# Performance work log

Measured on AMD Instinct MI355X. Metric: run time of the kernel, lower is better.

The kernel has to match this reference:

```python
import jax, jax.numpy as jnp
import numpy as np

N_NODES = 50000
N_EDGES = 800000


def _gcn_conv(x, src, dst, norm, W, b, num_nodes):
    # x: [N, Fin] -> h: [N, Fout]; messages gathered from src, scattered to dst.
    h = x @ W
    msgs = h[src] * norm[:, None]                      # [E+N, Fout]
    out = jax.ops.segment_sum(msgs, dst, num_segments=num_nodes)
    return out + b


def _gcn_norm(edge_index, num_nodes):
    # Add self-loops and compute symmetric normalization D^-1/2 (A+I) D^-1/2.
    loops = jnp.arange(num_nodes, dtype=edge_index.dtype)
    src = jnp.concatenate([edge_index[0], loops])
    dst = jnp.concatenate([edge_index[1], loops])
    ones = jnp.ones(src.shape[0], dtype=jnp.float32)
    deg = jax.ops.segment_sum(ones, dst, num_segments=num_nodes)
    dinv = jnp.where(deg > 0, jax.lax.rsqrt(jnp.maximum(deg, 1.0)), 0.0)
    norm = dinv[src] * dinv[dst]
    return src, dst, norm


def setup_inputs() -> dict:
    key = jax.random.key(0)
    k1, k2, k3, k4 = jax.random.split(key, 4)
    map_x = jax.random.normal(k1, (N_NODES, 128), dtype=jnp.float32)
    edge_index = jax.random.randint(k2, (2, N_EDGES), 0, N_NODES, dtype=jnp.int64)
    W1 = jax.random.normal(k3, (128, 64), dtype=jnp.float32) * (1.0 / np.sqrt(128))
    b1 = jnp.zeros((64,), dtype=jnp.float32)
    W2 = jax.random.normal(k4, (64, 32), dtype=jnp.float32) * (1.0 / np.sqrt(64))
    b2 = jnp.zeros((32,), dtype=jnp.float32)
    return {"map": map_x, "edge_index": edge_index, "W1": W1, "b1": b1, "W2": W2, "b2": b2}


def reference(map, edge_index, W1, b1, W2, b2):
    num_nodes = map.shape[0]
    src, dst, norm = _gcn_norm(edge_index, num_nodes)
    x = jax.nn.relu(_gcn_conv(map, src, dst, norm, W1, b1, num_nodes))
    x = jax.nn.relu(_gcn_conv(x, src, dst, norm, W2, b2, num_nodes))
    return x
```

## Files before the change

### kernel.cpp

```cpp
#include <hip/hip_runtime.h>

#define TPB 256
#define ACHUNK 4096
#define BSHIFT 6
#define BNODES 64
#define CAP 2048
#define GROWS 128

__device__ __forceinline__ float blo(unsigned u) { return __uint_as_float(u << 16); }
__device__ __forceinline__ float bhi(unsigned u) { return __uint_as_float(u & 0xffff0000u); }
__device__ __forceinline__ unsigned pack2(float a, float b) {
    unsigned ua = __float_as_uint(a); ua += 0x7fffu + ((ua >> 16) & 1u);
    unsigned ub = __float_as_uint(b); ub += 0x7fffu + ((ub >> 16) & 1u);
    return (ua >> 16) | (ub & 0xffff0000u);
}
__device__ __forceinline__ void dec8(uint4 v, float* f) {
    f[0] = blo(v.x); f[1] = bhi(v.x); f[2] = blo(v.y); f[3] = bhi(v.y);
    f[4] = blo(v.z); f[5] = bhi(v.z); f[6] = blo(v.w); f[7] = bhi(v.w);
}
__device__ __forceinline__ void dec4(uint2 v, float* f) {
    f[0] = blo(v.x); f[1] = bhi(v.x); f[2] = blo(v.y); f[3] = bhi(v.y);
}


__global__ __launch_bounds__(TPB) void k_fat(
        const int* __restrict__ src, const int* __restrict__ dst, int E,
        int* __restrict__ bcnt, int* __restrict__ tmp, int NB,
        const float* __restrict__ X, const float* __restrict__ W,
        unsigned int* __restrict__ H1b, int N, int G1, int FB) {
    __shared__ float Ws[128 * 64];
    int* lcnt = (int*)Ws;
    int bid = blockIdx.x;
    int t = threadIdx.x;

    if ((bid % 3) == 0) {
        int fidx = bid / 3;
        if (fidx >= FB) return;
        int c0 = fidx * ACHUNK;
        int s_[16], d_[16];
#pragma unroll
        for (int i = 0; i < 16; i++) {
            int e = c0 + i * TPB + t;
            if (e < E) { s_[i] = src[e]; d_[i] = dst[e]; }
            else d_[i] = -1;
        }
        for (int b = t; b < NB; b += TPB) lcnt[b] = 0;
        __syncthreads();
#pragma unroll
        for (int i = 0; i < 16; i++)
            if (d_[i] >= 0) atomicAdd(&lcnt[d_[i] >> BSHIFT], 1);
        __syncthreads();
        for (int b = t; b < NB; b += TPB) {
            int c = lcnt[b];
            lcnt[b] = c ? (b * CAP + atomicAdd(&bcnt[b], c)) : 0;
        }
        __syncthreads();
#pragma unroll
        for (int i = 0; i < 16; i++) {
            if (d_[i] >= 0) {
                int bkt = d_[i] >> BSHIFT;
                int pos = atomicAdd(&lcnt[bkt], 1);
                if (pos < (bkt + 1) * CAP) {
                    tmp[pos] = ((d_[i] & (BNODES - 1)) << 16) | s_[i];
                }
            }
        }
    } else {
        int gb = bid - bid / 3 - 1;
        if (gb >= G1) return;
        int row0 = gb * GROWS;

        const float4* W4 = (const float4*)W;
        float4* Ws4 = (float4*)Ws;
#pragma unroll
        for (int i = 0; i < 8; i++) Ws4[t + i * 256] = W4[t + i * 256];
        __syncthreads();

        int rg = t >> 3;
        int c0 = (t & 7) * 8;
        int r0 = row0 + rg * 4;
        int ri[4];
#pragma unroll
        for (int i = 0; i < 4; i++) ri[i] = (r0 + i < N) ? (r0 + i) : (N - 1);

        float acc[4][8];
#pragma unroll
        for (int i = 0; i < 4; i++)
#pragma unroll
            for (int j = 0; j < 8; j++) acc[i][j] = 0.0f;

        const float4* X4 = (const float4*)X;
        for (int kk = 0; kk < 32; kk++) {
            float4 xv[4];
#pragma unroll
            for (int i = 0; i < 4; i++) xv[i] = X4[(size_t)ri[i] * 32 + kk];
#pragma unroll
            for (int q = 0; q < 4; q++) {
                const float* w = Ws + (4 * kk + q) * 64 + c0;
                float wq[8];
#pragma unroll
                for (int j = 0; j < 8; j++) wq[j] = w[j];
                float xq[4];
                xq[0] = q == 0 ? xv[0].x : q == 1 ? xv[0].y : q == 2 ? xv[0].z : xv[0].w;
                xq[1] = q == 0 ? xv[1].x : q == 1 ? xv[1].y : q == 2 ? xv[1].z : xv[1].w;
                xq[2] = q == 0 ? xv[2].x : q == 1 ? xv[2].y : q == 2 ? xv[2].z : xv[2].w;
                xq[3] = q == 0 ? xv[3].x : q == 1 ? xv[3].y : q == 2 ? xv[3].z : xv[3].w;
#pragma unroll
                for (int i = 0; i < 4; i++)
#pragma unroll
                    for (int j = 0; j < 8; j++)
                        acc[i][j] = fmaf(xq[i], wq[j], acc[i][j]);
            }
        }
#pragma unroll
        for (int i = 0; i < 4; i++) {
            if (r0 + i < N) {
                uint4 p = { pack2(acc[i][0], acc[i][1]), pack2(acc[i][2], acc[i][3]),
                            pack2(acc[i][4], acc[i][5]), pack2(acc[i][6], acc[i][7]) };
                *(uint4*)(H1b + (size_t)(r0 + i) * 32 + (t & 7) * 4) = p;
            }
        }
    }
}


__global__ __launch_bounds__(TPB) void k_csr(
        const int* __restrict__ bcnt, const int* __restrict__ tmp,
        int* __restrict__ rowptr, unsigned short* __restrict__ rowlen,
        float* __restrict__ dinv, unsigned short* __restrict__ edges, int N) {
    __shared__ int hist[BNODES];
    __shared__ int cur[BNODES];
    __shared__ int sh[BNODES];
    int b = blockIdx.x;
    int t = threadIdx.x;
    int node0 = b << BSHIFT;
    int nn = N - node0; if (nn > BNODES) nn = BNODES;
    int cnt = bcnt[b]; if (cnt > CAP) cnt = CAP;
    const int tb = b * CAP;

    int v[8];
#pragma unroll
    for (int i = 0; i < 8; i++) {
        int idx = t + i * TPB;
        v[i] = (idx < cnt) ? tmp[tb + idx] : -1;
    }
    if (t < BNODES) hist[t] = 0;
    __syncthreads();
#pragma unroll
    for (int i = 0; i < 8; i++)
        if (v[i] >= 0) atomicAdd(&hist[v[i] >> 16], 1);
    __syncthreads();
    if (t < BNODES) sh[t] = (hist[t] + 7) & ~7;
    __syncthreads();
    for (int o = 1; o < BNODES; o <<= 1) {
        int x = (t >= o && t < BNODES) ? sh[t - o] : 0;
        __syncthreads();
        if (t < BNODES) sh[t] += x;
        __syncthreads();
    }
    if (t < BNODES) {
        int len = hist[t];
        int excl = sh[t] - ((len + 7) & ~7);
        cur[t] = excl;
        float dv = rsqrtf((float)(len + 1));
        if (t < nn) {
            dinv[node0 + t] = dv;
            rowptr[node0 + t] = tb + excl;
            rowlen[node0 + t] = (unsigned short)len;
        }
    }
    __syncthreads();
#pragma unroll
    for (int i = 0; i < 8; i++) {
        if (v[i] >= 0) {
            int pos = atomicAdd(&cur[v[i] >> 16], 1);
            if (pos < CAP)
                edges[tb + pos] = (unsigned short)(v[i] & 0xffff);
        }
    }
}


__global__ __launch_bounds__(TPB) void k_gg(
        const int* __restrict__ rowptr, const unsigned short* __restrict__ rowlen,
        const unsigned short* __restrict__ edges,
        const unsigned int* __restrict__ h1b,
        const float* __restrict__ dinv, const float* __restrict__ b1,
        const float* __restrict__ W2, unsigned int* __restrict__ g2b, int N) {
    __shared__ float W2s[64 * 32];
    __shared__ float rows[32 * 68];
    __shared__ float dl[32];
    __shared__ int nst[32];
    __shared__ int nlen[32];
    int t = threadIdx.x;
    int node0 = blockIdx.x * 32;
    int nn = N - node0; if (nn > 32) nn = 32;
    if (nn <= 0) return;

    {
        const float4* W4 = (const float4*)W2;
        float4* Wd = (float4*)W2s;
        Wd[t] = W4[t]; Wd[t + 256] = W4[t + 256];
    }
    if (t < nn) {
        dl[t] = dinv[node0 + t];
        nst[t] = rowptr[node0 + t];
        nlen[t] = rowlen[node0 + t];
    }
    __syncthreads();

    const uint4* G4 = (const uint4*)h1b;
    int nl = t >> 3;
    int lane = t & 7;
    if (nl < nn) {
        float acc[8], f[8];
        float w0 = dl[nl];
        uint4 sv = G4[(size_t)(node0 + nl) * 8 + lane];
        dec8(sv, f);
#pragma unroll
        for (int k = 0; k < 8; k++) acc[k] = w0 * f[k];
        int base = nst[nl], deg = nlen[nl];
        int j = 0;
        for (; j + 7 < deg; j += 8) {
            uint4 ev = *(const uint4*)(edges + base + j);
            int s[8];
            s[0] = ev.x & 0xffff; s[1] = ev.x >> 16;
            s[2] = ev.y & 0xffff; s[3] = ev.y >> 16;
            s[4] = ev.z & 0xffff; s[5] = ev.z >> 16;
            s[6] = ev.w & 0xffff; s[7] = ev.w >> 16;
            uint4 r[8]; float dv[8];
#pragma unroll
            for (int u = 0; u < 8; u++) {
                r[u] = G4[(size_t)s[u] * 8 + lane];
                dv[u] = dinv[s[u]];
            }
#pragma unroll
            for (int u = 0; u < 8; u++) {
                dec8(r[u], f);
#pragma unroll
                for (int k = 0; k < 8; k++) acc[k] = fmaf(dv[u], f[k], acc[k]);
            }
        }
        for (; j < deg; j++) {
            int s0 = edges[base + j];
            float dvx = dinv[s0];
            uint4 r0 = G4[(size_t)s0 * 8 + lane];
            dec8(r0, f);
#pragma unroll
            for (int k = 0; k < 8; k++) acc[k] = fmaf(dvx, f[k], acc[k]);
        }
        const float4* bb4 = (const float4*)(b1 + lane * 8);
        float4 ba = bb4[0], bc = bb4[1];
        float* rr = rows + nl * 68 + lane * 8;
        rr[0] = fmaxf(fmaf(acc[0], w0, ba.x), 0.0f);
        rr[1] = fmaxf(fmaf(acc[1], w0, ba.y), 0.0f);
        rr[2] = fmaxf(fmaf(acc[2], w0, ba.z), 0.0f);
        rr[3] = fmaxf(fmaf(acc[3], w0, ba.w), 0.0f);
        rr[4] = fmaxf(fmaf(acc[4], w0, bc.x), 0.0f);
        rr[5] = fmaxf(fmaf(acc[5], w0, bc.y), 0.0f);
        rr[6] = fmaxf(fmaf(acc[6], w0, bc.z), 0.0f);
        rr[7] = fmaxf(fmaf(acc[7], w0, bc.w), 0.0f);
    }
    __syncthreads();

    int n = t >> 3;
    int c = t & 7;
    if (n < nn) {
        const float* row = rows + n * 68;
        float a0 = 0.0f, a1 = 0.0f, a2 = 0.0f, a3 = 0.0f;
#pragma unroll 8
        for (int k = 0; k < 64; k++) {
            float rv = row[k];
            const float* w = W2s + k * 32 + 4 * c;
            a0 = fmaf(rv, w[0], a0); a1 = fmaf(rv, w[1], a1);
            a2 = fmaf(rv, w[2], a2); a3 = fmaf(rv, w[3], a3);
        }
        float dv = dl[n];
        uint2 p = { pack2(a0 * dv, a1 * dv), pack2(a2 * dv, a3 * dv) };
        ((uint2*)g2b)[(size_t)(node0 + n) * 8 + c] = p;
    }
}


__global__ __launch_bounds__(TPB) void k_g32(
        const int* __restrict__ rowptr, const unsigned short* __restrict__ rowlen,
        const unsigned short* __restrict__ edges,
        const unsigned int* __restrict__ g2b,
        const float* __restrict__ dinv, const float* __restrict__ b2,
        float* __restrict__ out, int N) {
    __shared__ float dl[32];
    __shared__ int nst[32];
    __shared__ int nlen[32];
    int t = threadIdx.x;
    int node0 = blockIdx.x * 32;
    int nn = N - node0; if (nn > 32) nn = 32;
    if (nn <= 0) return;
    if (t < nn) {
        dl[t] = dinv[node0 + t];
        nst[t] = rowptr[node0 + t];
        nlen[t] = rowlen[node0 + t];
    }
    __syncthreads();

    int nl = t >> 3;
    int lane = t & 7;
    if (nl >= nn) return;

    const uint2* G2 = (const uint2*)g2b;
    float acc[4], f[4];
    uint2 sv = G2[(size_t)(node0 + nl) * 8 + lane];
    dec4(sv, acc);
    int base = nst[nl], deg = nlen[nl];
    int j = 0;
    for (; j + 15 < deg; j += 16) {
        uint4 ea = *(const uint4*)(edges + base + j);
        uint4 eb = *(const uint4*)(edges + base + j + 8);
        int s[16];
        s[0]  = ea.x & 0xffff; s[1]  = ea.x >> 16; s[2]  = ea.y & 0xffff; s[3]  = ea.y >> 16;
        s[4]  = ea.z & 0xffff; s[5]  = ea.z >> 16; s[6]  = ea.w & 0xffff; s[7]  = ea.w >> 16;
        s[8]  = eb.x & 0xffff; s[9]  = eb.x >> 16; s[10] = eb.y & 0xffff; s[11] = eb.y >> 16;
        s[12] = eb.z & 0xffff; s[13] = eb.z >> 16; s[14] = eb.w & 0xffff; s[15] = eb.w >> 16;
        uint2 r[16];
#pragma unroll
        for (int u = 0; u < 16; u++) r[u] = G2[(size_t)s[u] * 8 + lane];
#pragma unroll
        for (int u = 0; u < 16; u++) {
            dec4(r[u], f);
            acc[0] += f[0]; acc[1] += f[1]; acc[2] += f[2]; acc[3] += f[3];
        }
    }
    for (; j + 7 < deg; j += 8) {
        uint4 ea = *(const uint4*)(edges + base + j);
        int s[8];
        s[0] = ea.x & 0xffff; s[1] = ea.x >> 16; s[2] = ea.y & 0xffff; s[3] = ea.y >> 16;
        s[4] = ea.z & 0xffff; s[5] = ea.z >> 16; s[6] = ea.w & 0xffff; s[7] = ea.w >> 16;
        uint2 r[8];
#pragma unroll
        for (int u = 0; u < 8; u++) r[u] = G2[(size_t)s[u] * 8 + lane];
#pragma unroll
        for (int u = 0; u < 8; u++) {
            dec4(r[u], f);
            acc[0] += f[0]; acc[1] += f[1]; acc[2] += f[2]; acc[3] += f[3];
        }
    }
    for (; j < deg; j++) {
        uint2 r0 = G2[(size_t)edges[base + j] * 8 + lane];
        dec4(r0, f);
        acc[0] += f[0]; acc[1] += f[1]; acc[2] += f[2]; acc[3] += f[3];
    }
    float w0 = dl[nl];
    const float4* bb4 = (const float4*)(b2 + lane * 4);
    float4 ba = bb4[0];
    float4 o0 = { fmaxf(fmaf(acc[0], w0, ba.x), 0.0f),
                  fmaxf(fmaf(acc[1], w0, ba.y), 0.0f),
                  fmaxf(fmaf(acc[2], w0, ba.z), 0.0f),
                  fmaxf(fmaf(acc[3], w0, ba.w), 0.0f) };
    *(float4*)(out + (size_t)(node0 + nl) * 32 + lane * 4) = o0;
}

static inline int cdiv(int a, int b) { return (a + b - 1) / b; }
static inline char* alignup(char* p) { return (char*)(((uintptr_t)p + 255) & ~(uintptr_t)255); }

extern "C" void kernel_launch(void* const* d_in, const int* in_sizes, int n_in,
                              void* d_out, int out_size, void* d_ws, size_t ws_size,
                              hipStream_t stream) {
    const float* x  = (const float*)d_in[0];
    const int*   ei = (const int*)d_in[1];
    const float* W1 = (const float*)d_in[2];
    const float* b1 = (const float*)d_in[3];
    const float* W2 = (const float*)d_in[4];
    const float* b2 = (const float*)d_in[5];
    float* out = (float*)d_out;

    int N = in_sizes[0] / 128;
    int E = in_sizes[1] / 2;
    const int* src = ei;
    const int* dst = ei + E;

    int NB = cdiv(N, BNODES);

    char* p = (char*)d_ws;
    float* dinv  = (float*)p;            p = alignup(p + sizeof(float) * N);
    int* rowptr  = (int*)p;              p = alignup(p + sizeof(int) * N);
    unsigned short* rowlen = (unsigned short*)p;  p = alignup(p + sizeof(short) * N);
    int* bcnt    = (int*)p;              p = alignup(p + sizeof(int) * 1024);
    int* tmp     = (int*)p;              p = alignup(p + sizeof(int) * (size_t)NB * CAP);
    unsigned short* edges = (unsigned short*)p;   p = alignup(p + sizeof(short) * (size_t)NB * CAP);
    unsigned int* h1b = (unsigned int*)p; p = alignup(p + sizeof(short) * (size_t)N * 64);
    unsigned int* g2b = (unsigned int*)p; p = alignup(p + sizeof(short) * (size_t)N * 32);

    dim3 blk(TPB);
    int FB = cdiv(E, ACHUNK);
    int G1 = cdiv(N, GROWS);
    int fat = 1;
    while ((fat + 2) / 3 < FB || fat - (fat + 2) / 3 < G1) fat++;

    hipMemsetAsync(bcnt, 0, sizeof(int) * 1024, stream);
    k_fat<<<fat, blk, 0, stream>>>(src, dst, E, bcnt, tmp, NB,
                                   x, W1, h1b, N, G1, FB);
    k_csr<<<NB, blk, 0, stream>>>(bcnt, tmp, rowptr, rowlen, dinv, edges, N);
    k_gg<<<cdiv(N, 32), blk, 0, stream>>>(rowptr, rowlen, edges, h1b,
                                          dinv, b1, W2, g2b, N);
    k_g32<<<cdiv(N, 32), blk, 0, stream>>>(rowptr, rowlen, edges, g2b,
                                           dinv, b2, out, N);
}
```

Baseline: 149.1 us.

## Fuse all GCN stages into one cooperative persistent kernel with grid syncs

Replaces the memset and four separate launches with a single cooperative kernel that loops over work items and uses grid-wide barriers between the bucketing/GEMM, CSR build, layer-1 gather, and layer-2 gather phases. Bucketing now writes per-chunk partitioned slots with private counts instead of global atomics on a shared counter, so no memset is needed and the CSR phase concatenates the chunk slices. This removes launch gaps and global atomics but adds grid.sync overhead and a persistent grid whose size comes from an occupancy query. The per-chunk cap of 64 edges per bucket could truncate edges on skewed inputs.

New measurement: 409.1 us. 174% more time.

```diff
diff --git a/kernel.cpp b/kernel.cpp
--- a/kernel.cpp
+++ b/kernel.cpp
@@ -1,11 +1,16 @@
 #include <hip/hip_runtime.h>
+#include <hip/hip_cooperative_groups.h>
+
+namespace cg = cooperative_groups;
 
 #define TPB 256
-#define ACHUNK 4096
+#define EPB 16384
 #define BSHIFT 6
 #define BNODES 64
+#define PCAP 64
 #define CAP 2048
 #define GROWS 128
+#define SMEMB 36864
 
 __device__ __forceinline__ float blo(unsigned u) { return __uint_as_float(u << 16); }
 __device__ __forceinline__ float bhi(unsigned u) { return __uint_as_float(u & 0xffff0000u); }
@@ -23,339 +28,361 @@
 }
 
 
-__global__ __launch_bounds__(TPB) void k_fat(
+__global__ __launch_bounds__(TPB, 4) void k_all(
         const int* __restrict__ src, const int* __restrict__ dst, int E,
-        int* __restrict__ bcnt, int* __restrict__ tmp, int NB,
-        const float* __restrict__ X, const float* __restrict__ W,
-        unsigned int* __restrict__ H1b, int N, int G1, int FB) {
-    __shared__ float Ws[128 * 64];
-    int* lcnt = (int*)Ws;
-    int bid = blockIdx.x;
-    int t = threadIdx.x;
-
-    if ((bid % 3) == 0) {
-        int fidx = bid / 3;
-        if (fidx >= FB) return;
-        int c0 = fidx * ACHUNK;
-        int s_[16], d_[16];
-#pragma unroll
-        for (int i = 0; i < 16; i++) {
-            int e = c0 + i * TPB + t;
-            if (e < E) { s_[i] = src[e]; d_[i] = dst[e]; }
-            else d_[i] = -1;
-        }
-        for (int b = t; b < NB; b += TPB) lcnt[b] = 0;
+        const float* __restrict__ X, const float* __restrict__ W1,
+        const float* __restrict__ b1, const float* __restrict__ W2,
+        const float* __restrict__ b2,
+        unsigned short* __restrict__ cnt, int* __restrict__ tmp,
+        float* __restrict__ dinv, int* __restrict__ rowptr,
+        unsigned short* __restrict__ rowlen, unsigned short* __restrict__ edges,
+        unsigned int* __restrict__ h1b, unsigned int* __restrict__ g2b,
+        float* __restrict__ out,
+        int N, int NB, int FB, int G1, int FAT, int NT) {
+    __shared__ __align__(16) char smem[SMEMB];
+    cg::grid_group grid = cg::this_grid();
+    const int t = threadIdx.x;
+    const int bid = blockIdx.x;
+    const int G = gridDim.x;
+
+    for (int w = bid; w < FAT; w += G) {
         __syncthreads();
-#pragma unroll
-        for (int i = 0; i < 16; i++)
-            if (d_[i] >= 0) atomicAdd(&lcnt[d_[i] >> BSHIFT], 1);
-        __syncthreads();
-        for (int b = t; b < NB; b += TPB) {
-            int c = lcnt[b];
-            lcnt[b] = c ? (b * CAP + atomicAdd(&bcnt[b], c)) : 0;
-        }
-        __syncthreads();
-#pragma unroll
-        for (int i = 0; i < 16; i++) {
-            if (d_[i] >= 0) {
-                int bkt = d_[i] >> BSHIFT;
-                int pos = atomicAdd(&lcnt[bkt], 1);
-                if (pos < (bkt + 1) * CAP) {
-                    tmp[pos] = ((d_[i] & (BNODES - 1)) << 16) | s_[i];
-                }
-            }
-        }
-    } else {
-        int gb = bid - bid / 3 - 1;
-        if (gb >= G1) return;
-        int row0 = gb * GROWS;
-
-        const float4* W4 = (const float4*)W;
-        float4* Ws4 = (float4*)Ws;
-#pragma unroll
-        for (int i = 0; i < 8; i++) Ws4[t + i * 256] = W4[t + i * 256];
-        __syncthreads();
-
-        int rg = t >> 3;
-        int c0 = (t & 7) * 8;
-        int r0 = row0 + rg * 4;
-        int ri[4];
-#pragma unroll
-        for (int i = 0; i < 4; i++) ri[i] = (r0 + i < N) ? (r0 + i) : (N - 1);
-
-        float acc[4][8];
-#pragma unroll
-        for (int i = 0; i < 4; i++)
-#pragma unroll
-            for (int j = 0; j < 8; j++) acc[i][j] = 0.0f;
-
-        const float4* X4 = (const float4*)X;
-        for (int kk = 0; kk < 32; kk++) {
-            float4 xv[4];
-#pragma unroll
-            for (int i = 0; i < 4; i++) xv[i] = X4[(size_t)ri[i] * 32 + kk];
-#pragma unroll
-            for (int q = 0; q < 4; q++) {
-                const float* w = Ws + (4 * kk + q) * 64 + c0;
-                float wq[8];
-#pragma unroll
-                for (int j = 0; j < 8; j++) wq[j] = w[j];
-                float xq[4];
-                xq[0] = q == 0 ? xv[0].x : q == 1 ? xv[0].y : q == 2 ? xv[0].z : xv[0].w;
-                xq[1] = q == 0 ? xv[1].x : q == 1 ? xv[1].y : q == 2 ? xv[1].z : xv[1].w;
-                xq[2] = q == 0 ? xv[2].x : q == 1 ? xv[2].y : q == 2 ? xv[2].z : xv[2].w;
-                xq[3] = q == 0 ? xv[3].x : q == 1 ? xv[3].y : q == 2 ? xv[3].z : xv[3].w;
+        if (w % 3 == 0) {
+            int k = w / 3;
+            if (k < FB) {
+                unsigned short* dstl = (unsigned short*)smem;
+                int* hist = (int*)(smem + 32768);
+                int e0 = k * EPB;
+                int ne = E - e0; if (ne > EPB) ne = EPB;
+                for (int b = t; b < NB; b += TPB) hist[b] = 0;
+                __syncthreads();
+                for (int i = t; i < ne; i += TPB) {
+                    int d = dst[e0 + i];
+                    dstl[i] = (unsigned short)d;
+                    atomicAdd(&hist[d >> BSHIFT], 1);
+                }
+                __syncthreads();
+                for (int b = t; b < NB; b += TPB) {
+                    int c = hist[b]; if (c > PCAP) c = PCAP;
+                    cnt[k * NB + b] = (unsigned short)c;
+                    hist[b] = (k * NB + b) * PCAP;
+                }
+                __syncthreads();
+                for (int i = t; i < ne; i += TPB) {
+                    int s = src[e0 + i];
+                    int d = dstl[i];
+                    int b = d >> BSHIFT;
+                    int pos = atomicAdd(&hist[b], 1);
+                    if (pos < (k * NB + b + 1) * PCAP)
+                        tmp[pos] = ((d & (BNODES - 1)) << 16) | s;
+                }
+            }
+        } else {
+            int gb = w - w / 3 - 1;
+            if (gb < G1) {
+                float* Ws = (float*)smem;
+                const float4* W4 = (const float4*)W1;
+                float4* Ws4 = (float4*)Ws;
+#pragma unroll
+                for (int i = 0; i < 8; i++) Ws4[t + i * 256] = W4[t + i * 256];
+                __syncthreads();
+
+                int row0 = gb * GROWS;
+                int rg = t >> 3;
+                int c0 = (t & 7) * 8;
+                int r0 = row0 + rg * 4;
+                int ri[4];
+#pragma unroll
+                for (int i = 0; i < 4; i++) ri[i] = (r0 + i < N) ? (r0 + i) : (N - 1);
+
+                float acc[4][8];
 #pragma unroll
                 for (int i = 0; i < 4; i++)
 #pragma unroll
-                    for (int j = 0; j < 8; j++)
-                        acc[i][j] = fmaf(xq[i], wq[j], acc[i][j]);
-            }
-        }
-#pragma unroll
-        for (int i = 0; i < 4; i++) {
-            if (r0 + i < N) {
-                uint4 p = { pack2(acc[i][0], acc[i][1]), pack2(acc[i][2], acc[i][3]),
-                            pack2(acc[i][4], acc[i][5]), pack2(acc[i][6], acc[i][7]) };
-                *(uint4*)(H1b + (size_t)(r0 + i) * 32 + (t & 7) * 4) = p;
+                    for (int j = 0; j < 8; j++) acc[i][j] = 0.0f;
+
+                const float4* X4 = (const float4*)X;
+                for (int kk = 0; kk < 32; kk++) {
+                    float4 xv[4];
+#pragma unroll
+                    for (int i = 0; i < 4; i++) xv[i] = X4[(size_t)ri[i] * 32 + kk];
+#pragma unroll
+                    for (int q = 0; q < 4; q++) {
+                        const float* ww = Ws + (4 * kk + q) * 64 + c0;
+                        float wq[8];
+#pragma unroll
+                        for (int j = 0; j < 8; j++) wq[j] = ww[j];
+                        float xq[4];
+                        xq[0] = q == 0 ? xv[0].x : q == 1 ? xv[0].y : q == 2 ? xv[0].z : xv[0].w;
+                        xq[1] = q == 0 ? xv[1].x : q == 1 ? xv[1].y : q == 2 ? xv[1].z : xv[1].w;
+                        xq[2] = q == 0 ? xv[2].x : q == 1 ? xv[2].y : q == 2 ? xv[2].z : xv[2].w;
+                        xq[3] = q == 0 ? xv[3].x : q == 1 ? xv[3].y : q == 2 ? xv[3].z : xv[3].w;
+#pragma unroll
+                        for (int i = 0; i < 4; i++)
+#pragma unroll
+                            for (int j = 0; j < 8; j++)
+                                acc[i][j] = fmaf(xq[i], wq[j], acc[i][j]);
+                    }
+                }
+#pragma unroll
+                for (int i = 0; i < 4; i++) {
+                    if (r0 + i < N) {
+                        uint4 p = { pack2(acc[i][0], acc[i][1]), pack2(acc[i][2], acc[i][3]),
+                                    pack2(acc[i][4], acc[i][5]), pack2(acc[i][6], acc[i][7]) };
+                        *(uint4*)(h1b + (size_t)(r0 + i) * 32 + (t & 7) * 4) = p;
+                    }
+                }
             }
         }
     }
-}
-
-
-__global__ __launch_bounds__(TPB) void k_csr(
-        const int* __restrict__ bcnt, const int* __restrict__ tmp,
-        int* __restrict__ rowptr, unsigned short* __restrict__ rowlen,
-        float* __restrict__ dinv, unsigned short* __restrict__ edges, int N) {
-    __shared__ int hist[BNODES];
-    __shared__ int cur[BNODES];
-    __shared__ int sh[BNODES];
-    int b = blockIdx.x;
-    int t = threadIdx.x;
-    int node0 = b << BSHIFT;
-    int nn = N - node0; if (nn > BNODES) nn = BNODES;
-    int cnt = bcnt[b]; if (cnt > CAP) cnt = CAP;
-    const int tb = b * CAP;
-
-    int v[8];
-#pragma unroll
-    for (int i = 0; i < 8; i++) {
-        int idx = t + i * TPB;
-        v[i] = (idx < cnt) ? tmp[tb + idx] : -1;
-    }
-    if (t < BNODES) hist[t] = 0;
-    __syncthreads();
-#pragma unroll
-    for (int i = 0; i < 8; i++)
-        if (v[i] >= 0) atomicAdd(&hist[v[i] >> 16], 1);
-    __syncthreads();
-    if (t < BNODES) sh[t] = (hist[t] + 7) & ~7;
-    __syncthreads();
-    for (int o = 1; o < BNODES; o <<= 1) {
-        int x = (t >= o && t < BNODES) ? sh[t - o] : 0;
-        __syncthreads();
-        if (t < BNODES) sh[t] += x;
-        __syncthreads();
-    }
-    if (t < BNODES) {
-        int len = hist[t];
-        int excl = sh[t] - ((len + 7) & ~7);
-        cur[t] = excl;
-        float dv = rsqrtf((float)(len + 1));
-        if (t < nn) {
-            dinv[node0 + t] = dv;
-            rowptr[node0 + t] = tb + excl;
-            rowlen[node0 + t] = (unsigned short)len;
+
+    grid.sync();
+
+    {
+        int* sl   = (int*)smem;
+        int* cc   = (int*)(smem + 8192);
+        int* offs = (int*)(smem + 8448);
+        int* hist = (int*)(smem + 8704);
+        int* cur  = (int*)(smem + 8960);
+        int* sh   = (int*)(smem + 9216);
+        for (int b = bid; b < NB; b += G) {
+            __syncthreads();
+            if (t < FB) cc[t] = cnt[t * NB + b];
+            __syncthreads();
+            if (t == 0) {
+                int o = 0;
+                for (int k = 0; k < FB; k++) { offs[k] = o; o += cc[k]; }
+                offs[FB] = (o > CAP) ? CAP : o;
+            }
+            __syncthreads();
+            {
+                int k = t / 5, j = t % 5;
+                if (k < FB) {
+                    int c = cc[k], o = offs[k];
+                    int gbase = (k * NB + b) * PCAP;
+                    for (int i = j; i < c; i += 5) {
+                        int p = o + i;
+                        if (p < CAP) sl[p] = tmp[gbase + i];
+                    }
+                }
+            }
+            __syncthreads();
+            int cntB = offs[FB];
+            int node0 = b << BSHIFT;
+            int nn = N - node0; if (nn > BNODES) nn = BNODES;
+            const int tb = b * CAP;
+
+            int v[8];
+#pragma unroll
+            for (int i = 0; i < 8; i++) {
+                int idx = t + i * TPB;
+                v[i] = (idx < cntB) ? sl[idx] : -1;
+            }
+            if (t < BNODES) hist[t] = 0;
+            __syncthreads();
+#pragma unroll
+            for (int i = 0; i < 8; i++)
+                if (v[i] >= 0) atomicAdd(&hist[v[i] >> 16], 1);
+            __syncthreads();
+            if (t < BNODES) sh[t] = (hist[t] + 7) & ~7;
+            __syncthreads();
+            for (int o = 1; o < BNODES; o <<= 1) {
+                int x = (t >= o && t < BNODES) ? sh[t - o] : 0;
+                __syncthreads();
+                if (t < BNODES) sh[t] += x;
+                __syncthreads();
+            }
+            if (t < BNODES) {
+                int len = hist[t];
+                int excl = sh[t] - ((len + 7) & ~7);
+                cur[t] = excl;
+                float dv = rsqrtf((float)(len + 1));
+                if (t < nn) {
+                    dinv[node0 + t] = dv;
+                    rowptr[node0 + t] = tb + excl;
+                    rowlen[node0 + t] = (unsigned short)len;
+                }
+            }
+            __syncthreads();
+#pragma unroll
+            for (int i = 0; i < 8; i++) {
+                if (v[i] >= 0) {
+                    int pos = atomicAdd(&cur[v[i] >> 16], 1);
+                    if (pos < CAP)
+                        edges[tb + pos] = (unsigned short)(v[i] & 0xffff);
+                }
+            }
         }
     }
-    __syncthreads();
-#pragma unroll
-    for (int i = 0; i < 8; i++) {
-        if (v[i] >= 0) {
-            int pos = atomicAdd(&cur[v[i] >> 16], 1);
-            if (pos < CAP)
-                edges[tb + pos] = (unsigned short)(v[i] & 0xffff);
+
+    grid.sync();
+
+    {
+        float* W2s  = (float*)smem;
+        float* rows = (float*)(smem + 8192);
+        float* dl   = (float*)(smem + 16896);
+        int* nst    = (int*)(smem + 17024);
+        int* nlen   = (int*)(smem + 17152);
+        {
+            const float4* W4 = (const float4*)W2;
+            float4* Wd = (float4*)W2s;
+            Wd[t] = W4[t]; Wd[t + 256] = W4[t + 256];
+        }
+        int lane = t & 7;
+        const float4* bb4 = (const float4*)(b1 + lane * 8);
+        float4 ba = bb4[0], bc = bb4[1];
+        __syncthreads();
+
+        const uint4* G4 = (const uint4*)h1b;
+        for (int tile = bid; tile < NT; tile += G) {
+            int node0 = tile * 32;
+            int nn = N - node0; if (nn > 32) nn = 32;
+            if (t < nn) {
+                dl[t] = dinv[node0 + t];
+                nst[t] = rowptr[node0 + t];
+                nlen[t] = rowlen[node0 + t];
+            }
+            __syncthreads();
+            int nl = t >> 3;
+            if (nl < nn) {
+                float acc[8], f[8];
+                float w0 = dl[nl];
+                uint4 sv = G4[(size_t)(node0 + nl) * 8 + lane];
+                dec8(sv, f);
+#pragma unroll
+                for (int k = 0; k < 8; k++) acc[k] = w0 * f[k];
+                int base = nst[nl], deg = nlen[nl];
+                int j = 0;
+                for (; j + 7 < deg; j += 8) {
+                    uint4 ev = *(const uint4*)(edges + base + j);
+                    int s[8];
+                    s[0] = ev.x & 0xffff; s[1] = ev.x >> 16;
+                    s[2] = ev.y & 0xffff; s[3] = ev.y >> 16;
+                    s[4] = ev.z & 0xffff; s[5] = ev.z >> 16;
+                    s[6] = ev.w & 0xffff; s[7] = ev.w >> 16;
+                    uint4 r[8]; float dv[8];
+#pragma unroll
+                    for (int u = 0; u < 8; u++) {
+                        r[u] = G4[(size_t)s[u] * 8 + lane];
+                        dv[u] = dinv[s[u]];
+                    }
+#pragma unroll
+                    for (int u = 0; u < 8; u++) {
+                        dec8(r[u], f);
+#pragma unroll
+                        for (int k = 0; k < 8; k++) acc[k] = fmaf(dv[u], f[k], acc[k]);
+                    }
+                }
+                for (; j < deg; j++) {
+                    int s0 = edges[base + j];
+                    float dvx = dinv[s0];
+                    uint4 r0 = G4[(size_t)s0 * 8 + lane];
+                    dec8(r0, f);
+#pragma unroll
+                    for (int k = 0; k < 8; k++) acc[k] = fmaf(dvx, f[k], acc[k]);
+                }
+                float* rr = rows + nl * 68 + lane * 8;
+                rr[0] = fmaxf(fmaf(acc[0], w0, ba.x), 0.0f);
+                rr[1] = fmaxf(fmaf(acc[1], w0, ba.y), 0.0f);
+                rr[2] = fmaxf(fmaf(acc[2], w0, ba.z), 0.0f);
+                rr[3] = fmaxf(fmaf(acc[3], w0, ba.w), 0.0f);
+                rr[4] = fmaxf(fmaf(acc[4], w0, bc.x), 0.0f);
+                rr[5] = fmaxf(fmaf(acc[5], w0, bc.y), 0.0f);
+                rr[6] = fmaxf(fmaf(acc[6], w0, bc.z), 0.0f);
+                rr[7] = fmaxf(fmaf(acc[7], w0, bc.w), 0.0f);
+            }
+            __syncthreads();
+            int n = t >> 3;
+            int c = t & 7;
+            if (n < nn) {
+                const float* row = rows + n * 68;
+                float a0 = 0.0f, a1 = 0.0f, a2 = 0.0f, a3 = 0.0f;
+#pragma unroll 8
+                for (int k = 0; k < 64; k++) {
+                    float rv = row[k];
+                    const float* ww = W2s + k * 32 + 4 * c;
+                    a0 = fmaf(rv, ww[0], a0); a1 = fmaf(rv, ww[1], a1);
+                    a2 = fmaf(rv, ww[2], a2); a3 = fmaf(rv, ww[3], a3);
+                }
+                float dv = dl[n];
+                uint2 p = { pack2(a0 * dv, a1 * dv), pack2(a2 * dv, a3 * dv) };
+                ((uint2*)g2b)[(size_t)(node0 + n) * 8 + c] = p;
+            }
+            __syncthreads();
         }
     }
-}
-
-
-__global__ __launch_bounds__(TPB) void k_gg(
-        const int* __restrict__ rowptr, const unsigned short* __restrict__ rowlen,
-        const unsigned short* __restrict__ edges,
-        const unsigned int* __restrict__ h1b,
-        const float* __restrict__ dinv, const float* __restrict__ b1,
-        const float* __restrict__ W2, unsigned int* __restrict__ g2b, int N) {
-    __shared__ float W2s[64 * 32];
-    __shared__ float rows[32 * 68];
-    __shared__ float dl[32];
-    __shared__ int nst[32];
-    __shared__ int nlen[32];
-    int t = threadIdx.x;
-    int node0 = blockIdx.x * 32;
-    int nn = N - node0; if (nn > 32) nn = 32;
-    if (nn <= 0) return;
+
+    grid.sync();
 
     {
-        const float4* W4 = (const float4*)W2;
-        float4* Wd = (float4*)W2s;
-        Wd[t] = W4[t]; Wd[t + 256] = W4[t + 256];
-    }
-    if (t < nn) {
-        dl[t] = dinv[node0 + t];
-        nst[t] = rowptr[node0 + t];
-        nlen[t] = rowlen[node0 + t];
-    }
-    __syncthreads();
-
-    const uint4* G4 = (const uint4*)h1b;
-    int nl = t >> 3;
-    int lane = t & 7;
-    if (nl < nn) {
-        float acc[8], f[8];
-        float w0 = dl[nl];
-        uint4 sv = G4[(size_t)(node0 + nl) * 8 + lane];
-        dec8(sv, f);
-#pragma unroll
-        for (int k = 0; k < 8; k++) acc[k] = w0 * f[k];
-        int base = nst[nl], deg = nlen[nl];
-        int j = 0;
-        for (; j + 7 < deg; j += 8) {
-            uint4 ev = *(const uint4*)(edges + base + j);
-            int s[8];
-            s[0] = ev.x & 0xffff; s[1] = ev.x >> 16;
-            s[2] = ev.y & 0xffff; s[3] = ev.y >> 16;
-            s[4] = ev.z & 0xffff; s[5] = ev.z >> 16;
-            s[6] = ev.w & 0xffff; s[7] = ev.w >> 16;
-            uint4 r[8]; float dv[8];
-#pragma unroll
-            for (int u = 0; u < 8; u++) {
-                r[u] = G4[(size_t)s[u] * 8 + lane];
-                dv[u] = dinv[s[u]];
-            }
-#pragma unroll
-            for (int u = 0; u < 8; u++) {
-                dec8(r[u], f);
-#pragma unroll
-                for (int k = 0; k < 8; k++) acc[k] = fmaf(dv[u], f[k], acc[k]);
-            }
-        }
-        for (; j < deg; j++) {
-            int s0 = edges[base + j];
-            float dvx = dinv[s0];
-            uint4 r0 = G4[(size_t)s0 * 8 + lane];
-            dec8(r0, f);
-#pragma unroll
-            for (int k = 0; k < 8; k++) acc[k] = fmaf(dvx, f[k], acc[k]);
-        }
-        const float4* bb4 = (const float4*)(b1 + lane * 8);
-        float4 ba = bb4[0], bc = bb4[1];
-        float* rr = rows + nl * 68 + lane * 8;
-        rr[0] = fmaxf(fmaf(acc[0], w0, ba.x), 0.0f);
-        rr[1] = fmaxf(fmaf(acc[1], w0, ba.y), 0.0f);
-        rr[2] = fmaxf(fmaf(acc[2], w0, ba.z), 0.0f);
-        rr[3] = fmaxf(fmaf(acc[3], w0, ba.w), 0.0f);
-        rr[4] = fmaxf(fmaf(acc[4], w0, bc.x), 0.0f);
-        rr[5] = fmaxf(fmaf(acc[5], w0, bc.y), 0.0f);
-        rr[6] = fmaxf(fmaf(acc[6], w0, bc.z), 0.0f);
-        rr[7] = fmaxf(fmaf(acc[7], w0, bc.w), 0.0f);
-    }
-    __syncthreads();
-
-    int n = t >> 3;
-    int c = t & 7;
-    if (n < nn) {
-        const float* row = rows + n * 68;
-        float a0 = 0.0f, a1 = 0.0f, a2 = 0.0f, a3 = 0.0f;
-#pragma unroll 8
-        for (int k = 0; k < 64; k++) {
-            float rv = row[k];
-            const float* w = W2s + k * 32 + 4 * c;
-            a0 = fmaf(rv, w[0], a0); a1 = fmaf(rv, w[1], a1);
-            a2 = fmaf(rv, w[2], a2); a3 = fmaf(rv, w[3], a3);
-        }
-        float dv = dl[n];
-        uint2 p = { pack2(a0 * dv, a1 * dv), pack2(a2 * dv, a3 * dv) };
-        ((uint2*)g2b)[(size_t)(node0 + n) * 8 + c] = p;
-    }
-}
-
-
-__global__ __launch_bounds__(TPB) void k_g32(
-        const int* __restrict__ rowptr, const unsigned short* __restrict__ rowlen,
-        const unsigned short* __restrict__ edges,
-        const unsigned int* __restrict__ g2b,
-        const float* __restrict__ dinv, const float* __restrict__ b2,
-        float* __restrict__ out, int N) {
-    __shared__ float dl[32];
-    __shared__ int nst[32];
-    __shared__ int nlen[32];
-    int t = threadIdx.x;
-    int node0 = blockIdx.x * 32;
-    int nn = N - node0; if (nn > 32) nn = 32;
-    if (nn <= 0) return;
-    if (t < nn) {
-        dl[t] = dinv[node0 + t];
-        nst[t] = rowptr[node0 + t];
-        nlen[t] = rowlen[node0 + t];
-    }
-    __syncthreads();
-
-    int nl = t >> 3;
-    int lane = t & 7;
-    if (nl >= nn) return;
-
-    const uint2* G2 = (const uint2*)g2b;
-    float acc[4], f[4];
-    uint2 sv = G2[(size_t)(node0 + nl) * 8 + lane];
-    dec4(sv, acc);
-    int base = nst[nl], deg = nlen[nl];
-    int j = 0;
-    for (; j + 15 < deg; j += 16) {
-        uint4 ea = *(const uint4*)(edges + base + j);
-        uint4 eb = *(const uint4*)(edges + base + j + 8);
-        int s[16];
-        s[0]  = ea.x & 0xffff; s[1]  = ea.x >> 16; s[2]  = ea.y & 0xffff; s[3]  = ea.y >> 16;
-        s[4]  = ea.z & 0xffff; s[5]  = ea.z >> 16; s[6]  = ea.w & 0xffff; s[7]  = ea.w >> 16;
-        s[8]  = eb.x & 0xffff; s[9]  = eb.x >> 16; s[10] = eb.y & 0xffff; s[11] = eb.y >> 16;
-        s[12] = eb.z & 0xffff; s[13] = eb.z >> 16; s[14] = eb.w & 0xffff; s[15] = eb.w >> 16;
-        uint2 r[16];
-#pragma unroll
-        for (int u = 0; u < 16; u++) r[u] = G2[(size_t)s[u] * 8 + lane];
-#pragma unroll
-        for (int u = 0; u < 16; u++) {
-            dec4(r[u], f);
-            acc[0] += f[0]; acc[1] += f[1]; acc[2] += f[2]; acc[3] += f[3];
+        float* dl = (float*)(smem + 16896);
+        int* nst  = (int*)(smem + 17024);
+        int* nlen = (int*)(smem + 17152);
+        const uint2* G2 = (const uint2*)g2b;
+        int lane = t & 7;
+        const float4 ba = *(const float4*)(b2 + lane * 4);
+        for (int tile = bid; tile < NT; tile += G) {
+            int node0 = tile * 32;
+            int nn = N - node0; if (nn > 32) nn = 32;
+            __syncthreads();
+            if (t < nn) {
+                dl[t] = dinv[node0 + t];
+                nst[t] = rowptr[node0 + t];
+                nlen[t] = rowlen[node0 + t];
+            }
+            __syncthreads();
+            int nl = t >> 3;
+            if (nl < nn) {
+                float acc[4], f[4];
+                uint2 sv = G2[(size_t)(node0 + nl) * 8 + lane];
+                dec4(sv, acc);
+                int base = nst[nl], deg = nlen[nl];
+                int j = 0;
+                for (; j + 15 < deg; j += 16) {
+                    uint4 ea = *(const uint4*)(edges + base + j);
+                    uint4 eb = *(const uint4*)(edges + base + j + 8);
+                    int s[16];
+                    s[0]  = ea.x & 0xffff; s[1]  = ea.x >> 16; s[2]  = ea.y & 0xffff; s[3]  = ea.y >> 16;
+                    s[4]  = ea.z & 0xffff; s[5]  = ea.z >> 16; s[6]  = ea.w & 0xffff; s[7]  = ea.w >> 16;
+                    s[8]  = eb.x & 0xffff; s[9]  = eb.x >> 16; s[10] = eb.y & 0xffff; s[11] = eb.y >> 16;
+                    s[12] = eb.z & 0xffff; s[13] = eb.z >> 16; s[14] = eb.w & 0xffff; s[15] = eb.w >> 16;
+                    uint2 r[16];
+#pragma unroll
+                    for (int u = 0; u < 16; u++) r[u] = G2[(size_t)s[u] * 8 + lane];
+#pragma unroll
+                    for (int u = 0; u < 16; u++) {
+                        dec4(r[u], f);
+                        acc[0] += f[0]; acc[1] += f[1]; acc[2] += f[2]; acc[3] += f[3];
+                    }
+                }
+                for (; j + 7 < deg; j += 8) {
+                    uint4 ea = *(const uint4*)(edges + base + j);
+                    int s[8];
+                    s[0] = ea.x & 0xffff; s[1] = ea.x >> 16; s[2] = ea.y & 0xffff; s[3] = ea.y >> 16;
+                    s[4] = ea.z & 0xffff; s[5] = ea.z >> 16; s[6] = ea.w & 0xffff; s[7] = ea.w >> 16;
+                    uint2 r[8];
+#pragma unroll
+                    for (int u = 0; u < 8; u++) r[u] = G2[(size_t)s[u] * 8 + lane];
+#pragma unroll
+                    for (int u = 0; u < 8; u++) {
+                        dec4(r[u], f);
+                        acc[0] += f[0]; acc[1] += f[1]; acc[2] += f[2]; acc[3] += f[3];
+                    }
+                }
+                for (; j < deg; j++) {
+                    uint2 r0 = G2[(size_t)edges[base + j] * 8 + lane];
+                    dec4(r0, f);
+                    acc[0] += f[0]; acc[1] += f[1]; acc[2] += f[2]; acc[3] += f[3];
+                }
+                float w0 = dl[nl];
+                float4 o0 = { fmaxf(fmaf(acc[0], w0, ba.x), 0.0f),
+                              fmaxf(fmaf(acc[1], w0, ba.y), 0.0f),
+                              fmaxf(fmaf(acc[2], w0, ba.z), 0.0f),
+                              fmaxf(fmaf(acc[3], w0, ba.w), 0.0f) };
+                *(float4*)(out + (size_t)(node0 + nl) * 32 + lane * 4) = o0;
+            }
         }
     }
-    for (; j + 7 < deg; j += 8) {
-        uint4 ea = *(const uint4*)(edges + base + j);
-        int s[8];
-        s[0] = ea.x & 0xffff; s[1] = ea.x >> 16; s[2] = ea.y & 0xffff; s[3] = ea.y >> 16;
-        s[4] = ea.z & 0xffff; s[5] = ea.z >> 16; s[6] = ea.w & 0xffff; s[7] = ea.w >> 16;
-        uint2 r[8];
-#pragma unroll
-        for (int u = 0; u < 8; u++) r[u] = G2[(size_t)s[u] * 8 + lane];
-#pragma unroll
-        for (int u = 0; u < 8; u++) {
-            dec4(r[u], f);
-            acc[0] += f[0]; acc[1] += f[1]; acc[2] += f[2]; acc[3] += f[3];
-        }
-    }
-    for (; j < deg; j++) {
-        uint2 r0 = G2[(size_t)edges[base + j] * 8 + lane];
-        dec4(r0, f);
-        acc[0] += f[0]; acc[1] += f[1]; acc[2] += f[2]; acc[3] += f[3];
-    }
-    float w0 = dl[nl];
-    const float4* bb4 = (const float4*)(b2 + lane * 4);
-    float4 ba = bb4[0];
-    float4 o0 = { fmaxf(fmaf(acc[0], w0, ba.x), 0.0f),
-                  fmaxf(fmaf(acc[1], w0, ba.y), 0.0f),
-                  fmaxf(fmaf(acc[2], w0, ba.z), 0.0f),
-                  fmaxf(fmaf(acc[3], w0, ba.w), 0.0f) };
-    *(float4*)(out + (size_t)(node0 + nl) * 32 + lane * 4) = o0;
 }
 
 static inline int cdiv(int a, int b) { return (a + b - 1) / b; }
@@ -378,29 +405,41 @@
     const int* dst = ei + E;
 
     int NB = cdiv(N, BNODES);
+    int FB = cdiv(E, EPB);
+    int G1 = cdiv(N, GROWS);
+    int NT = cdiv(N, 32);
+    int FAT = 1;
+    while ((FAT + 2) / 3 < FB || FAT - (FAT + 2) / 3 < G1) FAT++;
 
     char* p = (char*)d_ws;
     float* dinv  = (float*)p;            p = alignup(p + sizeof(float) * N);
     int* rowptr  = (int*)p;              p = alignup(p + sizeof(int) * N);
     unsigned short* rowlen = (unsigned short*)p;  p = alignup(p + sizeof(short) * N);
-    int* bcnt    = (int*)p;              p = alignup(p + sizeof(int) * 1024);
-    int* tmp     = (int*)p;              p = alignup(p + sizeof(int) * (size_t)NB * CAP);
+    unsigned short* cnt = (unsigned short*)p;     p = alignup(p + sizeof(short) * (size_t)FB * NB);
+    int* tmp     = (int*)p;              p = alignup(p + sizeof(int) * (size_t)FB * NB * PCAP);
     unsigned short* edges = (unsigned short*)p;   p = alignup(p + sizeof(short) * (size_t)NB * CAP);
     unsigned int* h1b = (unsigned int*)p; p = alignup(p + sizeof(short) * (size_t)N * 64);
     unsigned int* g2b = (unsigned int*)p; p = alignup(p + sizeof(short) * (size_t)N * 32);
 
-    dim3 blk(TPB);
-    int FB = cdiv(E, ACHUNK);
-    int G1 = cdiv(N, GROWS);
-    int fat = 1;
-    while ((fat + 2) / 3 < FB || fat - (fat + 2) / 3 < G1) fat++;
-
-    hipMemsetAsync(bcnt, 0, sizeof(int) * 1024, stream);
-    k_fat<<<fat, blk, 0, stream>>>(src, dst, E, bcnt, tmp, NB,
-                                   x, W1, h1b, N, G1, FB);
-    k_csr<<<NB, blk, 0, stream>>>(bcnt, tmp, rowptr, rowlen, dinv, edges, N);
-    k_gg<<<cdiv(N, 32), blk, 0, stream>>>(rowptr, rowlen, edges, h1b,
-                                          dinv, b1, W2, g2b, N);
-    k_g32<<<cdiv(N, 32), blk, 0, stream>>>(rowptr, rowlen, edges, g2b,
-                                           dinv, b2, out, N);
+    static int g_blocks = -1;
+    if (g_blocks < 0) {
+        int mb = 0;
+        hipOccupancyMaxActiveBlocksPerMultiprocessor(&mb, k_all, TPB, 0);
+        if (mb < 1) mb = 1;
+        hipDeviceProp_t prop;
+        int dev = 0;
+        hipGetDevice(&dev);
+        hipGetDeviceProperties(&prop, dev);
+        g_blocks = mb * prop.multiProcessorCount;
+        if (g_blocks < 1) g_blocks = 256;
+    }
+    int G = g_blocks;
+
+    void* args[] = { (void*)&src, (void*)&dst, (void*)&E,
+                     (void*)&x, (void*)&W1, (void*)&b1, (void*)&W2, (void*)&b2,
+                     (void*)&cnt, (void*)&tmp, (void*)&dinv, (void*)&rowptr,
+                     (void*)&rowlen, (void*)&edges, (void*)&h1b, (void*)&g2b,
+                     (void*)&out, (void*)&N, (void*)&NB, (void*)&FB, (void*)&G1,
+                     (void*)&FAT, (void*)&NT };
+    hipLaunchCooperativeKernel((void*)k_all, dim3(G), dim3(TPB), args, 0, stream);
 }
```

## Replace global bucket atomics with per-chunk bucket slots and in-block compaction

Applied to the files above, without the earlier changes.

The edge-bucketing pass now gives each (chunk, bucket) pair its own fixed-size slot of PCAP entries and records a per-slot count. This replaces the global atomicAdd on bucket counters and removes the memset that zeroed them. The CSR kernel runs a block-wide prefix scan over the per-chunk counts, then gathers the slot contents into shared memory before building the histogram. The trade-off is a larger, sparser temporary buffer and less coalesced gathered reads in k_csr. It also assumes FB fits in one block (at most 256 chunks) and that no chunk puts more than PCAP edges into one bucket.

Result: slower. 152.2 us (+2.0%).

```diff
diff --git a/kernel.cpp b/kernel.cpp
--- a/kernel.cpp
+++ b/kernel.cpp
@@ -4,6 +4,7 @@
 #define ACHUNK 4096
 #define BSHIFT 6
 #define BNODES 64
+#define PCAP 32
 #define CAP 2048
 #define GROWS 128
 
@@ -25,7 +26,7 @@
 
 __global__ __launch_bounds__(TPB) void k_fat(
         const int* __restrict__ src, const int* __restrict__ dst, int E,
-        int* __restrict__ bcnt, int* __restrict__ tmp, int NB,
+        unsigned short* __restrict__ cnt, int* __restrict__ tmp, int NB,
         const float* __restrict__ X, const float* __restrict__ W,
         unsigned int* __restrict__ H1b, int N, int G1, int FB) {
     __shared__ float Ws[128 * 64];
@@ -34,9 +35,9 @@
     int t = threadIdx.x;
 
     if ((bid % 3) == 0) {
-        int fidx = bid / 3;
-        if (fidx >= FB) return;
-        int c0 = fidx * ACHUNK;
+        int k = bid / 3;
+        if (k >= FB) return;
+        int c0 = k * ACHUNK;
         int s_[16], d_[16];
 #pragma unroll
         for (int i = 0; i < 16; i++) {
@@ -51,8 +52,9 @@
             if (d_[i] >= 0) atomicAdd(&lcnt[d_[i] >> BSHIFT], 1);
         __syncthreads();
         for (int b = t; b < NB; b += TPB) {
-            int c = lcnt[b];
-            lcnt[b] = c ? (b * CAP + atomicAdd(&bcnt[b], c)) : 0;
+            int c = lcnt[b]; if (c > PCAP) c = PCAP;
+            cnt[k * NB + b] = (unsigned short)c;
+            lcnt[b] = (k * NB + b) * PCAP;
         }
         __syncthreads();
 #pragma unroll
@@ -60,9 +62,8 @@
             if (d_[i] >= 0) {
                 int bkt = d_[i] >> BSHIFT;
                 int pos = atomicAdd(&lcnt[bkt], 1);
-                if (pos < (bkt + 1) * CAP) {
+                if (pos < (k * NB + bkt + 1) * PCAP)
                     tmp[pos] = ((d_[i] & (BNODES - 1)) << 16) | s_[i];
-                }
             }
         }
     } else {
@@ -125,9 +126,12 @@
 
 
 __global__ __launch_bounds__(TPB) void k_csr(
-        const int* __restrict__ bcnt, const int* __restrict__ tmp,
+        const unsigned short* __restrict__ cnt, const int* __restrict__ tmp,
         int* __restrict__ rowptr, unsigned short* __restrict__ rowlen,
-        float* __restrict__ dinv, unsigned short* __restrict__ edges, int N) {
+        float* __restrict__ dinv, unsigned short* __restrict__ edges,
+        int N, int NB, int FB) {
+    __shared__ int sl[CAP];
+    __shared__ int cc[TPB];
     __shared__ int hist[BNODES];
     __shared__ int cur[BNODES];
     __shared__ int sh[BNODES];
@@ -135,14 +139,34 @@
     int t = threadIdx.x;
     int node0 = b << BSHIFT;
     int nn = N - node0; if (nn > BNODES) nn = BNODES;
-    int cnt = bcnt[b]; if (cnt > CAP) cnt = CAP;
     const int tb = b * CAP;
+
+    int myc = 0;
+    if (t < FB) myc = cnt[t * NB + b];
+    cc[t] = myc;
+    __syncthreads();
+    for (int o = 1; o < TPB; o <<= 1) {
+        int x = (t >= o) ? cc[t - o] : 0;
+        __syncthreads();
+        cc[t] += x;
+        __syncthreads();
+    }
+    int total = cc[TPB - 1]; if (total > CAP) total = CAP;
+    int off = cc[t] - myc;
+    if (t < FB) {
+        int gbase = (t * NB + b) * PCAP;
+        for (int i = 0; i < myc; i++) {
+            int p = off + i;
+            if (p < CAP) sl[p] = tmp[gbase + i];
+        }
+    }
+    __syncthreads();
 
     int v[8];
 #pragma unroll
     for (int i = 0; i < 8; i++) {
         int idx = t + i * TPB;
-        v[i] = (idx < cnt) ? tmp[tb + idx] : -1;
+        v[i] = (idx < total) ? sl[idx] : -1;
     }
     if (t < BNODES) hist[t] = 0;
     __syncthreads();
@@ -378,27 +402,26 @@
     const int* dst = ei + E;
 
     int NB = cdiv(N, BNODES);
+    int FB = cdiv(E, ACHUNK);
+    int G1 = cdiv(N, GROWS);
 
     char* p = (char*)d_ws;
     float* dinv  = (float*)p;            p = alignup(p + sizeof(float) * N);
     int* rowptr  = (int*)p;              p = alignup(p + sizeof(int) * N);
     unsigned short* rowlen = (unsigned short*)p;  p = alignup(p + sizeof(short) * N);
-    int* bcnt    = (int*)p;              p = alignup(p + sizeof(int) * 1024);
-    int* tmp     = (int*)p;              p = alignup(p + sizeof(int) * (size_t)NB * CAP);
+    unsigned short* cnt = (unsigned short*)p;     p = alignup(p + sizeof(short) * (size_t)FB * NB);
+    int* tmp     = (int*)p;              p = alignup(p + sizeof(int) * (size_t)FB * NB * PCAP);
     unsigned short* edges = (unsigned short*)p;   p = alignup(p + sizeof(short) * (size_t)NB * CAP);
     unsigned int* h1b = (unsigned int*)p; p = alignup(p + sizeof(short) * (size_t)N * 64);
     unsigned int* g2b = (unsigned int*)p; p = alignup(p + sizeof(short) * (size_t)N * 32);
 
     dim3 blk(TPB);
-    int FB = cdiv(E, ACHUNK);
-    int G1 = cdiv(N, GROWS);
     int fat = 1;
     while ((fat + 2) / 3 < FB || fat - (fat + 2) / 3 < G1) fat++;
 
-    hipMemsetAsync(bcnt, 0, sizeof(int) * 1024, stream);
-    k_fat<<<fat, blk, 0, stream>>>(src, dst, E, bcnt, tmp, NB,
+    k_fat<<<fat, blk, 0, stream>>>(src, dst, E, cnt, tmp, NB,
                                    x, W1, h1b, N, G1, FB);
-    k_csr<<<NB, blk, 0, stream>>>(bcnt, tmp, rowptr, rowlen, dinv, edges, N);
+    k_csr<<<NB, blk, 0, stream>>>(cnt, tmp, rowptr, rowlen, dinv, edges, N, NB, FB);
     k_gg<<<cdiv(N, 32), blk, 0, stream>>>(rowptr, rowlen, edges, h1b,
                                           dinv, b1, W2, g2b, N);
     k_g32<<<cdiv(N, 32), blk, 0, stream>>>(rowptr, rowlen, edges, g2b,
```

## Compute first-layer feature transform with bf16 MFMA instead of scalar FMAs

Applied to the files above, without the earlier changes.

Replaces the scalar fp32 FMA tile in the X@W1 path of the fused kernel with bf16 MFMA 16x16x32 instructions. X rows and the transposed W are converted to bf16 and staged in padded shared memory. Results are written back through shared memory so each thread emits coalesced bf16 stores. This cuts ALU work, but it enlarges shared memory to about 51KB, which may lower occupancy for the co-scheduled bucketing blocks, and it rounds the inputs to bf16 before the multiply.

Measured after the change: 138.1 us. -7.4%, faster.

```diff
diff --git a/kernel.cpp b/kernel.cpp
--- a/kernel.cpp
+++ b/kernel.cpp
@@ -6,6 +6,10 @@
 #define BNODES 64
 #define CAP 2048
 #define GROWS 128
+#define SMEMB 52224
+
+typedef __attribute__((ext_vector_type(8))) short bf16x8;
+typedef __attribute__((ext_vector_type(4))) float f32x4;
 
 __device__ __forceinline__ float blo(unsigned u) { return __uint_as_float(u << 16); }
 __device__ __forceinline__ float bhi(unsigned u) { return __uint_as_float(u & 0xffff0000u); }
@@ -28,12 +32,12 @@
         int* __restrict__ bcnt, int* __restrict__ tmp, int NB,
         const float* __restrict__ X, const float* __restrict__ W,
         unsigned int* __restrict__ H1b, int N, int G1, int FB) {
-    __shared__ float Ws[128 * 64];
-    int* lcnt = (int*)Ws;
+    __shared__ __align__(16) char smem[SMEMB];
     int bid = blockIdx.x;
     int t = threadIdx.x;
 
     if ((bid % 3) == 0) {
+        int* lcnt = (int*)smem;
         int fidx = bid / 3;
         if (fidx >= FB) return;
         int c0 = fidx * ACHUNK;
@@ -70,55 +74,83 @@
         if (gb >= G1) return;
         int row0 = gb * GROWS;
 
-        const float4* W4 = (const float4*)W;
-        float4* Ws4 = (float4*)Ws;
-#pragma unroll
-        for (int i = 0; i < 8; i++) Ws4[t + i * 256] = W4[t + i * 256];
-        __syncthreads();
-
-        int rg = t >> 3;
-        int c0 = (t & 7) * 8;
-        int r0 = row0 + rg * 4;
-        int ri[4];
-#pragma unroll
-        for (int i = 0; i < 4; i++) ri[i] = (r0 + i < N) ? (r0 + i) : (N - 1);
-
-        float acc[4][8];
-#pragma unroll
-        for (int i = 0; i < 4; i++)
-#pragma unroll
-            for (int j = 0; j < 8; j++) acc[i][j] = 0.0f;
+        unsigned int* XsU32 = (unsigned int*)smem;
+        unsigned int* WtU32 = (unsigned int*)(smem + 34816);
+        const unsigned short* XsU = (const unsigned short*)smem;
+        const unsigned short* WtU = (const unsigned short*)(smem + 34816);
 
         const float4* X4 = (const float4*)X;
-        for (int kk = 0; kk < 32; kk++) {
-            float4 xv[4];
-#pragma unroll
-            for (int i = 0; i < 4; i++) xv[i] = X4[(size_t)ri[i] * 32 + kk];
-#pragma unroll
-            for (int q = 0; q < 4; q++) {
-                const float* w = Ws + (4 * kk + q) * 64 + c0;
-                float wq[8];
-#pragma unroll
-                for (int j = 0; j < 8; j++) wq[j] = w[j];
-                float xq[4];
-                xq[0] = q == 0 ? xv[0].x : q == 1 ? xv[0].y : q == 2 ? xv[0].z : xv[0].w;
-                xq[1] = q == 0 ? xv[1].x : q == 1 ? xv[1].y : q == 2 ? xv[1].z : xv[1].w;
-                xq[2] = q == 0 ? xv[2].x : q == 1 ? xv[2].y : q == 2 ? xv[2].z : xv[2].w;
-                xq[3] = q == 0 ? xv[3].x : q == 1 ? xv[3].y : q == 2 ? xv[3].z : xv[3].w;
-#pragma unroll
-                for (int i = 0; i < 4; i++)
-#pragma unroll
-                    for (int j = 0; j < 8; j++)
-                        acc[i][j] = fmaf(xq[i], wq[j], acc[i][j]);
+#pragma unroll
+        for (int i = 0; i < 16; i++) {
+            int q = t + i * 256;
+            int r = q >> 5, c4 = q & 31;
+            int gr = row0 + r; if (gr >= N) gr = N - 1;
+            float4 v = X4[(size_t)gr * 32 + c4];
+            unsigned int* dptr = XsU32 + r * 68 + c4 * 2;
+            dptr[0] = pack2(v.x, v.y);
+            dptr[1] = pack2(v.z, v.w);
+        }
+#pragma unroll
+        for (int i = 0; i < 16; i++) {
+            int q = t + i * 256;
+            int col = q & 63, kp = q >> 6;
+            float w0 = W[(size_t)(2 * kp) * 64 + col];
+            float w1 = W[(size_t)(2 * kp + 1) * 64 + col];
+            WtU32[col * 68 + kp] = pack2(w0, w1);
+        }
+        __syncthreads();
+
+        int lane = t & 63;
+        int wv = t >> 6;
+        int l15 = lane & 15;
+        int lg = lane >> 4;
+        f32x4 zero = {0.0f, 0.0f, 0.0f, 0.0f};
+        f32x4 acc[2][4];
+#pragma unroll
+        for (int mt = 0; mt < 2; mt++)
+#pragma unroll
+            for (int nt = 0; nt < 4; nt++) acc[mt][nt] = zero;
+
+#pragma unroll
+        for (int kk = 0; kk < 4; kk++) {
+            int ko = kk * 32 + lg * 8;
+            bf16x8 a0 = *reinterpret_cast<const bf16x8*>(XsU + (wv * 32 + l15) * 136 + ko);
+            bf16x8 a1 = *reinterpret_cast<const bf16x8*>(XsU + (wv * 32 + 16 + l15) * 136 + ko);
+            bf16x8 b[4];
+#pragma unroll
+            for (int nt = 0; nt < 4; nt++)
+                b[nt] = *reinterpret_cast<const bf16x8*>(WtU + (nt * 16 + l15) * 136 + ko);
+#pragma unroll
+            for (int nt = 0; nt < 4; nt++) {
+                acc[0][nt] = __builtin_amdgcn_mfma_f32_16x16x32_bf16(a0, b[nt], acc[0][nt], 0, 0, 0);
+                acc[1][nt] = __builtin_amdgcn_mfma_f32_16x16x32_bf16(a1, b[nt], acc[1][nt], 0, 0, 0);
             }
         }
-#pragma unroll
-        for (int i = 0; i < 4; i++) {
-            if (r0 + i < N) {
-                uint4 p = { pack2(acc[i][0], acc[i][1]), pack2(acc[i][2], acc[i][3]),
-                            pack2(acc[i][4], acc[i][5]), pack2(acc[i][6], acc[i][7]) };
-                *(uint4*)(H1b + (size_t)(r0 + i) * 32 + (t & 7) * 4) = p;
-            }
+        __syncthreads();
+
+        float* rows = (float*)smem;
+#pragma unroll
+        for (int mt = 0; mt < 2; mt++)
+#pragma unroll
+            for (int nt = 0; nt < 4; nt++)
+#pragma unroll
+                for (int r = 0; r < 4; r++)
+                    rows[(wv * 32 + mt * 16 + lg * 4 + r) * 68 + nt * 16 + l15] = acc[mt][nt][r];
+        __syncthreads();
+
+        int rr = t >> 1, hh = t & 1;
+        int grow = row0 + rr;
+        if (grow < N) {
+            const float* sp = rows + rr * 68 + hh * 32;
+            unsigned int u[16];
+#pragma unroll
+            for (int j = 0; j < 16; j++) u[j] = pack2(sp[2 * j], sp[2 * j + 1]);
+            uint4* dp = (uint4*)(H1b + (size_t)grow * 32 + hh * 16);
+            uint4 p0 = { u[0], u[1], u[2], u[3] };
+            uint4 p1 = { u[4], u[5], u[6], u[7] };
+            uint4 p2 = { u[8], u[9], u[10], u[11] };
+            uint4 p3 = { u[12], u[13], u[14], u[15] };
+            dp[0] = p0; dp[1] = p1; dp[2] = p2; dp[3] = p3;
         }
     }
 }
```
